# Kernel optimization log

Hardware: AMD Instinct MI355X
Metric: run time of the kernel (lower is better)

Reference implementation:

```python
import jax, jax.numpy as jnp
import numpy as np

HIDDEN = 1024
NUM_HEADS = 16
HEAD_SIZE = HIDDEN // NUM_HEADS
B, S = 2, 2048


def setup_inputs() -> dict:
    key = jax.random.key(0)
    k_x, k_wqkv, k_bqkv, k_wo, k_bo = jax.random.split(key, 5)
    x = jax.random.normal(k_x, (B, S, HIDDEN), dtype=jnp.float32)
    # Dense kernels, fan-in scaled like lecun_normal init
    Wqkv = jax.random.normal(k_wqkv, (HIDDEN, 3 * HIDDEN), dtype=jnp.float32) / np.sqrt(HIDDEN)
    bqkv = jnp.zeros((3 * HIDDEN,), dtype=jnp.float32)
    Wo = jax.random.normal(k_wo, (HIDDEN, HIDDEN), dtype=jnp.float32) / np.sqrt(HIDDEN)
    bo = jnp.zeros((HIDDEN,), dtype=jnp.float32)
    return {"x": x, "Wqkv": Wqkv, "bqkv": bqkv, "Wo": Wo, "bo": bo}


def reference(x, Wqkv, bqkv, Wo, bo):
    b, s, h = x.shape
    qkv = jnp.einsum('bsh,hf->bsf', x, Wqkv) + bqkv          # [b, s, 3*h]
    qkv = qkv.reshape(b, s, 3, NUM_HEADS, HEAD_SIZE)
    q, k, v = qkv[:, :, 0], qkv[:, :, 1], qkv[:, :, 2]        # [b, s, nh, hd]
    scale = 1.0 / np.sqrt(HEAD_SIZE)
    scores = jnp.einsum('bqhd,bkhd->bhqk', q, k) * scale      # [b, nh, s, s]
    weights = jax.nn.softmax(scores, axis=-1)
    attn = jnp.einsum('bhqk,bkhd->bqhd', weights, v)          # [b, s, nh, hd]
    attn = attn.reshape(b, s, h)
    return jnp.einsum('bsh,hf->bsf', attn, Wo) + bo
```

## Files before the change

kernel.cpp:

```cpp
#include <hip/hip_runtime.h>
#include <hip/hip_bf16.h>

#define HIDDEN 1024
#define NH 16
#define BATCH 2
#define SEQ 2048

typedef __attribute__((ext_vector_type(8))) short bf16x8;
typedef __attribute__((ext_vector_type(4))) float f32x4;

__device__ __forceinline__ ushort f2bf(float f) {
    __hip_bfloat16 h = __float2bfloat16(f);
    return *reinterpret_cast<ushort*>(&h);
}
__device__ __forceinline__ float bf2f(ushort u) {
    __hip_bfloat16 h;
    *reinterpret_cast<ushort*>(&h) = u;
    return __bfloat162float(h);
}

__device__ __forceinline__ void async_copy16(const ushort* g, ushort* l) {
    __builtin_amdgcn_global_load_lds((const __attribute__((address_space(1))) void*)g,
                                     (__attribute__((address_space(3))) void*)l,
                                     16, 0, 0);
}

__global__ void prep_kernel(const float* __restrict__ x,
                            const float* __restrict__ Wqkv,
                            const float* __restrict__ Wo,
                            ushort* __restrict__ xb,
                            ushort* __restrict__ Wt,
                            ushort* __restrict__ WoT_hi,
                            ushort* __restrict__ WoT_lo)
{
    __shared__ float t[32][33];
    const int bid = blockIdx.x;
    const int tid = threadIdx.x;

    if (bid < 4096) {
        int i = (bid * 256 + tid) * 4;
        float4 v = *(const float4*)(x + i);
        ushort4 w;
        w.x = f2bf(v.x); w.y = f2bf(v.y); w.z = f2bf(v.z); w.w = f2bf(v.w);
        *(ushort4*)(xb + i) = w;
        return;
    }
    const int r = tid >> 3;
    const int c = (tid & 7) * 4;
    if (bid < 7168) {
        int tt = bid - 4096;
        int k0 = (tt & 31) * 32;
        int n0 = (tt >> 5) * 32;
        const int N = 3 * HIDDEN, K = HIDDEN;
        float4 v = *(const float4*)(Wqkv + (size_t)(k0 + r) * N + n0 + c);
        t[r][c] = v.x; t[r][c + 1] = v.y; t[r][c + 2] = v.z; t[r][c + 3] = v.w;
        __syncthreads();
        ushort4 w;
        w.x = f2bf(t[c + 0][r]); w.y = f2bf(t[c + 1][r]);
        w.z = f2bf(t[c + 2][r]); w.w = f2bf(t[c + 3][r]);
        *(ushort4*)(Wt + (size_t)(n0 + r) * K + k0 + c) = w;
    } else {
        int tt = bid - 7168;
        int k0 = (tt & 31) * 32;
        int n0 = (tt >> 5) * 32;
        const int N = HIDDEN, K = HIDDEN;
        float4 v = *(const float4*)(Wo + (size_t)(k0 + r) * N + n0 + c);
        t[r][c] = v.x; t[r][c + 1] = v.y; t[r][c + 2] = v.z; t[r][c + 3] = v.w;
        __syncthreads();
        ushort4 whi, wlo;
        float vv;
        vv = t[c + 0][r]; whi.x = f2bf(vv); wlo.x = f2bf(vv - bf2f(whi.x));
        vv = t[c + 1][r]; whi.y = f2bf(vv); wlo.y = f2bf(vv - bf2f(whi.y));
        vv = t[c + 2][r]; whi.z = f2bf(vv); wlo.z = f2bf(vv - bf2f(whi.z));
        vv = t[c + 3][r]; whi.w = f2bf(vv); wlo.w = f2bf(vv - bf2f(whi.w));
        *(ushort4*)(WoT_hi + (size_t)(n0 + r) * K + k0 + c) = whi;
        *(ushort4*)(WoT_lo + (size_t)(n0 + r) * K + k0 + c) = wlo;
    }
}

__global__ void transpose_v_kernel(const ushort* __restrict__ qkvb,
                                   ushort* __restrict__ vtg)
{
    __shared__ ushort T[64][72];
    int blk = blockIdx.x;
    int st = blk & 31;
    int h  = (blk >> 5) & 15;
    int b  = blk >> 9;
    int s0 = st * 64;

    int s  = threadIdx.x >> 2;
    int c0 = (threadIdx.x & 3) * 2;
    const ushort* src = qkvb + ((size_t)(b * SEQ + s0 + s)) * 3072 + 2048 + h * 64;
    *(uint4*)&T[s][c0 * 8]     = *(const uint4*)(src + c0 * 8);
    *(uint4*)&T[s][c0 * 8 + 8] = *(const uint4*)(src + c0 * 8 + 8);
    __syncthreads();

    int d = threadIdx.x >> 2;
    ushort* dst = vtg + ((size_t)((b * NH + h) * 64 + d)) * SEQ + s0;
    #pragma unroll
    for (int cc = 0; cc < 2; cc++) {
        int c2 = (threadIdx.x & 3) * 2 + cc;
        ushort tmp[8];
        #pragma unroll
        for (int j = 0; j < 8; j++) {
            int sp = c2 * 8 + j;
            int key = (sp & 3) * 16 + (sp >> 2);
            tmp[j] = T[key][d];
        }
        *(uint4*)(dst + c2 * 8) = *(const uint4*)tmp;
    }
}

__global__ __launch_bounds__(256, 3)
void gemm_mfma_bf16_kernel(const ushort* __restrict__ A,
                           const ushort* __restrict__ Bt,
                           const float* __restrict__ bias,
                           ushort* __restrict__ C, int N,
                           int qscale_cols)
{
    constexpr int K = 1024;
    __shared__ ushort As[128 * 64];
    __shared__ ushort Bs[128 * 64];

    const int tid  = threadIdx.x;
    const int wave = tid >> 6;
    const int lane = tid & 63;
    const int l16  = lane & 15;
    const int quad = lane >> 4;
    const int wm = wave & 1, wn = wave >> 1;

    const int bm = blockIdx.y * 128;
    const int bn = blockIdx.x * 128;

    const int srow = lane >> 3;
    const int lblk = (lane & 7) ^ srow;
    const ushort* Ag = A  + (size_t)(bm + wave * 32 + srow) * K + lblk * 8;
    const ushort* Bg = Bt + (size_t)(bn + wave * 32 + srow) * K + lblk * 8;
    ushort* Asl = As + wave * 32 * 64;
    ushort* Bsl = Bs + wave * 32 * 64;

    f32x4 acc[4][4];
    #pragma unroll
    for (int i = 0; i < 4; i++)
        #pragma unroll
        for (int j = 0; j < 4; j++) acc[i][j] = (f32x4){0.f, 0.f, 0.f, 0.f};

    for (int k0 = 0; k0 < K; k0 += 64) {
        __syncthreads();
        #pragma unroll
        for (int t = 0; t < 4; t++) {
            async_copy16(Ag + (size_t)t * 8 * K + k0, Asl + t * 8 * 64);
            async_copy16(Bg + (size_t)t * 8 * K + k0, Bsl + t * 8 * 64);
        }
        __syncthreads();

        #pragma unroll
        for (int s = 0; s < 2; s++) {
            bf16x8 af[4], bfr[4];
            #pragma unroll
            for (int i = 0; i < 4; i++) {
                int m = wm * 64 + i * 16 + l16;
                int n = wn * 64 + i * 16 + l16;
                af[i]  = *(const bf16x8*)&As[m * 64 + (((s * 4 + quad) ^ (m & 7)) << 3)];
                bfr[i] = *(const bf16x8*)&Bs[n * 64 + (((s * 4 + quad) ^ (n & 7)) << 3)];
            }
            #pragma unroll
            for (int i = 0; i < 4; i++)
                #pragma unroll
                for (int j = 0; j < 4; j++)
                    acc[i][j] = __builtin_amdgcn_mfma_f32_16x16x32_bf16(af[i], bfr[j], acc[i][j], 0, 0, 0);
        }
    }

    #pragma unroll
    for (int j = 0; j < 4; j++) {
        int col = bn + wn * 64 + j * 16 + l16;
        float bv = bias[col];
        float s = (col < qscale_cols) ? 0.125f : 1.0f;
        #pragma unroll
        for (int i = 0; i < 4; i++) {
            int row0 = bm + wm * 64 + i * 16 + quad * 4;
            #pragma unroll
            for (int r = 0; r < 4; r++)
                C[(size_t)(row0 + r) * N + col] = f2bf((acc[i][j][r] + bv) * s);
        }
    }
}

__global__ __launch_bounds__(256, 2)
void gemm3_split_kernel(const ushort* __restrict__ Ahi,
                        const ushort* __restrict__ Alo,
                        const ushort* __restrict__ Bthi,
                        const ushort* __restrict__ Btlo,
                        const float* __restrict__ bias,
                        float* __restrict__ C)
{
    constexpr int K = 1024, N = 1024;
    __shared__ ushort AsHi[128 * 64];
    __shared__ ushort AsLo[128 * 64];
    __shared__ ushort BsHi[64 * 64];
    __shared__ ushort BsLo[64 * 64];

    const int tid  = threadIdx.x;
    const int wave = tid >> 6;
    const int lane = tid & 63;
    const int l16  = lane & 15;
    const int quad = lane >> 4;
    const int wm = wave & 1, wn = wave >> 1;

    const int bm = blockIdx.y * 128;
    const int bn = blockIdx.x * 64;

    const int srow = lane >> 3;
    const int lblk = (lane & 7) ^ srow;
    const size_t aoff = (size_t)(bm + wave * 32 + srow) * K + lblk * 8;
    const size_t boff = (size_t)(bn + wave * 16 + srow) * K + lblk * 8;
    const ushort* AgHi = Ahi + aoff;
    const ushort* AgLo = Alo + aoff;
    const ushort* BgHi = Bthi + boff;
    const ushort* BgLo = Btlo + boff;
    ushort* AslHi = AsHi + wave * 32 * 64;
    ushort* AslLo = AsLo + wave * 32 * 64;
    ushort* BslHi = BsHi + wave * 16 * 64;
    ushort* BslLo = BsLo + wave * 16 * 64;

    f32x4 acc[4][2];
    #pragma unroll
    for (int i = 0; i < 4; i++)
        #pragma unroll
        for (int j = 0; j < 2; j++) acc[i][j] = (f32x4){0.f, 0.f, 0.f, 0.f};

    for (int k0 = 0; k0 < K; k0 += 64) {
        __syncthreads();
        #pragma unroll
        for (int t = 0; t < 4; t++) {
            async_copy16(AgHi + (size_t)t * 8 * K + k0, AslHi + t * 8 * 64);
            async_copy16(AgLo + (size_t)t * 8 * K + k0, AslLo + t * 8 * 64);
        }
        #pragma unroll
        for (int t = 0; t < 2; t++) {
            async_copy16(BgHi + (size_t)t * 8 * K + k0, BslHi + t * 8 * 64);
            async_copy16(BgLo + (size_t)t * 8 * K + k0, BslLo + t * 8 * 64);
        }
        __syncthreads();

        #pragma unroll
        for (int s = 0; s < 2; s++) {
            bf16x8 ah[4], al[4], bh[2], bl[2];
            #pragma unroll
            for (int i = 0; i < 4; i++) {
                int m = wm * 64 + i * 16 + l16;
                int idx = m * 64 + (((s * 4 + quad) ^ (m & 7)) << 3);
                ah[i] = *(const bf16x8*)&AsHi[idx];
                al[i] = *(const bf16x8*)&AsLo[idx];
            }
            #pragma unroll
            for (int j = 0; j < 2; j++) {
                int n = wn * 32 + j * 16 + l16;
                int idx = n * 64 + (((s * 4 + quad) ^ (n & 7)) << 3);
                bh[j] = *(const bf16x8*)&BsHi[idx];
                bl[j] = *(const bf16x8*)&BsLo[idx];
            }
            #pragma unroll
            for (int i = 0; i < 4; i++)
                #pragma unroll
                for (int j = 0; j < 2; j++) {
                    acc[i][j] = __builtin_amdgcn_mfma_f32_16x16x32_bf16(ah[i], bh[j], acc[i][j], 0, 0, 0);
                    acc[i][j] = __builtin_amdgcn_mfma_f32_16x16x32_bf16(ah[i], bl[j], acc[i][j], 0, 0, 0);
                    acc[i][j] = __builtin_amdgcn_mfma_f32_16x16x32_bf16(al[i], bh[j], acc[i][j], 0, 0, 0);
                }
        }
    }

    #pragma unroll
    for (int j = 0; j < 2; j++) {
        int col = bn + wn * 32 + j * 16 + l16;
        float bv = bias[col];
        #pragma unroll
        for (int i = 0; i < 4; i++) {
            int row0 = bm + wm * 64 + i * 16 + quad * 4;
            #pragma unroll
            for (int r = 0; r < 4; r++)
                C[(size_t)(row0 + r) * N + col] = acc[i][j][r] + bv;
        }
    }
}

__global__ __launch_bounds__(256, 2)
void attn_mfma_kernel(const ushort* __restrict__ qkvb,
                      const ushort* __restrict__ vtg,
                      int use_vtg,
                      ushort* __restrict__ attn_hi,
                      ushort* __restrict__ attn_lo)
{
    __shared__ ushort Ks[2][64 * 64];
    __shared__ ushort Vs[2][64 * 64];
    __shared__ ushort Ps[4][32 * 72];

    const int tid  = threadIdx.x;
    const int wave = tid >> 6;
    const int lane = tid & 63;
    const int l16  = lane & 15;
    const int quad = lane >> 4;

    const int qb = blockIdx.x & 15;
    const int bh = blockIdx.x >> 4;
    const int h  = bh & (NH - 1);
    const int b  = bh >> 4;

    const int qbase = qb * 128;
    const int hoff  = h * 64;

    bf16x8 a_q[2][2];
    #pragma unroll
    for (int mg = 0; mg < 2; mg++) {
        int qrow = b * SEQ + qbase + wave * 32 + mg * 16 + l16;
        const ushort* qp = qkvb + (size_t)qrow * 3072 + hoff + quad * 8;
        a_q[mg][0] = *(const bf16x8*)qp;
        a_q[mg][1] = *(const bf16x8*)(qp + 32);
    }

    f32x4 o[2][4];
    f32x4 lacc[2];
    #pragma unroll
    for (int mg = 0; mg < 2; mg++) {
        lacc[mg] = (f32x4){0.f, 0.f, 0.f, 0.f};
        #pragma unroll
        for (int nt = 0; nt < 4; nt++) o[mg][nt] = (f32x4){0.f, 0.f, 0.f, 0.f};
    }

    bf16x8 b_ones;
    #pragma unroll
    for (int j = 0; j < 8; j++) b_ones[j] = (short)0x3f80;

    const ushort* kvb    = qkvb + (size_t)b * SEQ * 3072;
    const ushort* vtg_bh = vtg + (size_t)((b * NH + h) * 64) * SEQ;

    const int srow8 = lane >> 3;
    const int sblk  = lane & 7;
    const int gblk  = (sblk ^ srow8) << 3;
    const ushort* kg = kvb + (size_t)(wave * 16 + srow8) * 3072 + 1024 + hoff + gblk;
    const ushort* vg = vtg_bh + (size_t)(wave * 16 + srow8) * SEQ + gblk;

    if (use_vtg) {
        #pragma unroll
        for (int c = 0; c < 2; c++) {
            async_copy16(kg + (size_t)(c * 8) * 3072, &Ks[0][(wave * 16 + c * 8) * 64]);
            async_copy16(vg + (size_t)(c * 8) * SEQ,  &Vs[0][(wave * 16 + c * 8) * 64]);
        }
    }

    for (int t = 0; t < SEQ / 64; t++) {
        const int k0 = t * 64;
        const int cur = t & 1;

        if (use_vtg) {
            asm volatile("s_waitcnt vmcnt(0)" ::: "memory");
            asm volatile("s_barrier" ::: "memory");
            if (t < SEQ / 64 - 1) {
                const int nk0 = k0 + 64;
                #pragma unroll
                for (int c = 0; c < 2; c++) {
                    async_copy16(kg + (size_t)(nk0 + c * 8) * 3072,
                                 &Ks[cur ^ 1][(wave * 16 + c * 8) * 64]);
                    async_copy16(vg + (size_t)(c * 8) * SEQ + nk0,
                                 &Vs[cur ^ 1][(wave * 16 + c * 8) * 64]);
                }
            }
        } else {
            __syncthreads();
            #pragma unroll
            for (int i = 0; i < 2; i++) {
                int key = (tid >> 3) + 32 * i;
                int blk = tid & 7;
                const ushort* ksrc = kvb + (size_t)(k0 + key) * 3072 + 1024 + hoff + blk * 8;
                uint4 kv = *(const uint4*)ksrc;
                *(uint4*)&Ks[cur][key * 64 + ((blk ^ (key & 7)) << 3)] = kv;
                uint4 vv = *(const uint4*)(ksrc + 1024);
                const ushort* vp = (const ushort*)&vv;
                int pk_ = (key & 15) * 4 + (key >> 4);
                #pragma unroll
                for (int j = 0; j < 8; j++) {
                    int d = blk * 8 + j;
                    Vs[cur][d * 64 + (((pk_ >> 3) ^ (d & 7)) << 3) + (pk_ & 7)] = vp[j];
                }
            }
            __syncthreads();
        }

        f32x4 sc[2][4];
        #pragma unroll
        for (int nt = 0; nt < 4; nt++) {
            int key = nt * 16 + l16;
            bf16x8 bk0 = *(const bf16x8*)&Ks[cur][key * 64 + ((quad ^ (key & 7)) << 3)];
            bf16x8 bk1 = *(const bf16x8*)&Ks[cur][key * 64 + (((4 + quad) ^ (key & 7)) << 3)];
            #pragma unroll
            for (int mg = 0; mg < 2; mg++) {
                f32x4 a = (f32x4){0.f, 0.f, 0.f, 0.f};
                a = __builtin_amdgcn_mfma_f32_16x16x32_bf16(a_q[mg][0], bk0, a, 0, 0, 0);
                a = __builtin_amdgcn_mfma_f32_16x16x32_bf16(a_q[mg][1], bk1, a, 0, 0, 0);
                sc[mg][nt] = a;
            }
        }

        #pragma unroll
        for (int mg = 0; mg < 2; mg++) {
            #pragma unroll
            for (int r = 0; r < 4; r++) {
                int q = mg * 16 + quad * 4 + r;
                uint2 pk2;
                pk2.x = (uint)f2bf(__expf(sc[mg][0][r])) |
                        ((uint)f2bf(__expf(sc[mg][1][r])) << 16);
                pk2.y = (uint)f2bf(__expf(sc[mg][2][r])) |
                        ((uint)f2bf(__expf(sc[mg][3][r])) << 16);
                *(uint2*)&Ps[wave][q * 72 + l16 * 4] = pk2;
            }
        }

        asm volatile("s_waitcnt lgkmcnt(0)" ::: "memory");
        bf16x8 a_p[2][2];
        #pragma unroll
        for (int mg = 0; mg < 2; mg++) {
            a_p[mg][0] = *(const bf16x8*)&Ps[wave][(mg * 16 + l16) * 72 + quad * 8];
            a_p[mg][1] = *(const bf16x8*)&Ps[wave][(mg * 16 + l16) * 72 + 32 + quad * 8];
        }

        #pragma unroll
        for (int nt = 0; nt < 4; nt++) {
            int d = nt * 16 + l16;
            bf16x8 bv0 = *(const bf16x8*)&Vs[cur][d * 64 + ((quad ^ (d & 7)) << 3)];
            bf16x8 bv1 = *(const bf16x8*)&Vs[cur][d * 64 + (((4 + quad) ^ (d & 7)) << 3)];
            #pragma unroll
            for (int mg = 0; mg < 2; mg++) {
                o[mg][nt] = __builtin_amdgcn_mfma_f32_16x16x32_bf16(a_p[mg][0], bv0, o[mg][nt], 0, 0, 0);
                o[mg][nt] = __builtin_amdgcn_mfma_f32_16x16x32_bf16(a_p[mg][1], bv1, o[mg][nt], 0, 0, 0);
            }
        }
        #pragma unroll
        for (int mg = 0; mg < 2; mg++) {
            lacc[mg] = __builtin_amdgcn_mfma_f32_16x16x32_bf16(a_p[mg][0], b_ones, lacc[mg], 0, 0, 0);
            lacc[mg] = __builtin_amdgcn_mfma_f32_16x16x32_bf16(a_p[mg][1], b_ones, lacc[mg], 0, 0, 0);
        }
    }

    #pragma unroll
    for (int mg = 0; mg < 2; mg++) {
        #pragma unroll
        for (int r = 0; r < 4; r++) {
            float inv = 1.f / lacc[mg][r];
            int row = b * SEQ + qbase + wave * 32 + mg * 16 + quad * 4 + r;
            size_t base = (size_t)row * HIDDEN + hoff + l16;
            #pragma unroll
            for (int nt = 0; nt < 4; nt++) {
                float val = o[mg][nt][r] * inv;
                ushort hi = f2bf(val);
                ushort lo = f2bf(val - bf2f(hi));
                attn_hi[base + nt * 16] = hi;
                attn_lo[base + nt * 16] = lo;
            }
        }
    }
}

extern "C" void kernel_launch(void* const* d_in, const int* in_sizes, int n_in,
                              void* d_out, int out_size, void* d_ws, size_t ws_size,
                              hipStream_t stream) {
    const float* x    = (const float*)d_in[0];
    const float* Wqkv = (const float*)d_in[1];
    const float* bqkv = (const float*)d_in[2];
    const float* Wo   = (const float*)d_in[3];
    const float* bo   = (const float*)d_in[4];
    float* out = (float*)d_out;

    const int M = BATCH * SEQ;
    const size_t MB = 1024 * 1024;

    char* ws = (char*)d_ws;
    ushort* qkvb    = (ushort*)ws;
    ushort* attn_hi = (ushort*)(ws + 24 * MB);
    ushort* attn_lo = (ushort*)(ws + 32 * MB);
    ushort* xb      = (ushort*)(ws + 24 * MB);
    ushort* Wt      = (ushort*)(ws + 32 * MB);
    ushort* WoT_hi  = (ushort*)(ws + 40 * MB);
    ushort* WoT_lo  = (ushort*)(ws + 42 * MB);
    ushort* vtg     = (ushort*)(ws + 44 * MB);
    const int use_vtg = (ws_size >= 52 * MB) ? 1 : 0;

    prep_kernel<<<8192, 256, 0, stream>>>(x, Wqkv, Wo, xb, Wt, WoT_hi, WoT_lo);

    {
        dim3 grid((3 * HIDDEN) / 128, M / 128);
        gemm_mfma_bf16_kernel<<<grid, 256, 0, stream>>>(xb, Wt, bqkv, qkvb,
                                                        3 * HIDDEN, HIDDEN);
    }

    if (use_vtg) {
        transpose_v_kernel<<<BATCH * NH * (SEQ / 64), 256, 0, stream>>>(qkvb, vtg);
    }

    attn_mfma_kernel<<<BATCH * NH * (SEQ / 128), 256, 0, stream>>>(qkvb, vtg, use_vtg,
                                                                   attn_hi, attn_lo);

    {
        dim3 grid(HIDDEN / 64, M / 128);
        gemm3_split_kernel<<<grid, 256, 0, stream>>>(attn_hi, attn_lo,
                                                     WoT_hi, WoT_lo, bo, out);
    }
}
```

Baseline: 207.1 us.

## Split attention key range across two wave groups with LDS reduction

The attention kernel now launches 512 threads per block: two groups of four waves each process half of the key sequence for the same 128 queries. Afterwards they combine their partial O and row-sum accumulators through shared memory before normalizing and writing. The aim is to double the number of waves working on each query block, adding latency hiding and parallelism. In exchange it drops the double-buffered async prefetch, adds an extra barrier on every tile plus a final reduction, and raises occupancy demands through launch_bounds(512,4). Using unnormalized exp with no running max is unchanged from before.

```diff
diff --git a/kernel.cpp b/kernel.cpp
--- a/kernel.cpp
+++ b/kernel.cpp
@@ -286,22 +286,22 @@
     }
 }
 
-__global__ __launch_bounds__(256, 2)
+__global__ __launch_bounds__(512, 4)
 void attn_mfma_kernel(const ushort* __restrict__ qkvb,
                       const ushort* __restrict__ vtg,
                       int use_vtg,
                       ushort* __restrict__ attn_hi,
                       ushort* __restrict__ attn_lo)
 {
-    __shared__ ushort Ks[2][64 * 64];
-    __shared__ ushort Vs[2][64 * 64];
-    __shared__ ushort Ps[4][32 * 72];
-
-    const int tid  = threadIdx.x;
-    const int wave = tid >> 6;
-    const int lane = tid & 63;
-    const int l16  = lane & 15;
-    const int quad = lane >> 4;
+    __shared__ __align__(16) ushort smem[34816];
+
+    const int tid   = threadIdx.x;
+    const int wave  = tid >> 6;
+    const int wavel = wave & 3;
+    const int kh    = wave >> 2;
+    const int lane  = tid & 63;
+    const int l16   = lane & 15;
+    const int quad  = lane >> 4;
 
     const int qb = blockIdx.x & 15;
     const int bh = blockIdx.x >> 4;
@@ -311,10 +311,14 @@
     const int qbase = qb * 128;
     const int hoff  = h * 64;
 
+    ushort* KsH = smem + kh * 4096;
+    ushort* VsH = smem + 8192 + kh * 4096;
+    ushort* Psw = smem + 16384 + wave * 2304;
+
     bf16x8 a_q[2][2];
     #pragma unroll
     for (int mg = 0; mg < 2; mg++) {
-        int qrow = b * SEQ + qbase + wave * 32 + mg * 16 + l16;
+        int qrow = b * SEQ + qbase + wavel * 32 + mg * 16 + l16;
         const ushort* qp = qkvb + (size_t)qrow * 3072 + hoff + quad * 8;
         a_q[mg][0] = *(const bf16x8*)qp;
         a_q[mg][1] = *(const bf16x8*)(qp + 32);
@@ -337,63 +341,46 @@
     const ushort* vtg_bh = vtg + (size_t)((b * NH + h) * 64) * SEQ;
 
     const int srow8 = lane >> 3;
-    const int sblk  = lane & 7;
-    const int gblk  = (sblk ^ srow8) << 3;
-    const ushort* kg = kvb + (size_t)(wave * 16 + srow8) * 3072 + 1024 + hoff + gblk;
-    const ushort* vg = vtg_bh + (size_t)(wave * 16 + srow8) * SEQ + gblk;
-
-    if (use_vtg) {
-        #pragma unroll
-        for (int c = 0; c < 2; c++) {
-            async_copy16(kg + (size_t)(c * 8) * 3072, &Ks[0][(wave * 16 + c * 8) * 64]);
-            async_copy16(vg + (size_t)(c * 8) * SEQ,  &Vs[0][(wave * 16 + c * 8) * 64]);
-        }
-    }
-
-    for (int t = 0; t < SEQ / 64; t++) {
+    const int gblk  = ((lane & 7) ^ srow8) << 3;
+    const ushort* kg = kvb + (size_t)(kh * 1024 + wavel * 16 + srow8) * 3072 + 1024 + hoff + gblk;
+    const ushort* vg = vtg_bh + (size_t)(wavel * 16 + srow8) * SEQ + kh * 1024 + gblk;
+
+    for (int t = 0; t < 16; t++) {
         const int k0 = t * 64;
-        const int cur = t & 1;
-
+        __syncthreads();
         if (use_vtg) {
-            asm volatile("s_waitcnt vmcnt(0)" ::: "memory");
-            asm volatile("s_barrier" ::: "memory");
-            if (t < SEQ / 64 - 1) {
-                const int nk0 = k0 + 64;
-                #pragma unroll
-                for (int c = 0; c < 2; c++) {
-                    async_copy16(kg + (size_t)(nk0 + c * 8) * 3072,
-                                 &Ks[cur ^ 1][(wave * 16 + c * 8) * 64]);
-                    async_copy16(vg + (size_t)(c * 8) * SEQ + nk0,
-                                 &Vs[cur ^ 1][(wave * 16 + c * 8) * 64]);
-                }
+            #pragma unroll
+            for (int c = 0; c < 2; c++) {
+                async_copy16(kg + (size_t)(k0 + c * 8) * 3072, KsH + (wavel * 16 + c * 8) * 64);
+                async_copy16(vg + (size_t)(c * 8) * SEQ + k0,  VsH + (wavel * 16 + c * 8) * 64);
             }
         } else {
-            __syncthreads();
+            const int tl = tid & 255;
             #pragma unroll
             for (int i = 0; i < 2; i++) {
-                int key = (tid >> 3) + 32 * i;
-                int blk = tid & 7;
-                const ushort* ksrc = kvb + (size_t)(k0 + key) * 3072 + 1024 + hoff + blk * 8;
+                int key = (tl >> 3) + 32 * i;
+                int blk = tl & 7;
+                const ushort* ksrc = kvb + (size_t)(kh * 1024 + k0 + key) * 3072 + 1024 + hoff + blk * 8;
                 uint4 kv = *(const uint4*)ksrc;
-                *(uint4*)&Ks[cur][key * 64 + ((blk ^ (key & 7)) << 3)] = kv;
+                *(uint4*)&KsH[key * 64 + ((blk ^ (key & 7)) << 3)] = kv;
                 uint4 vv = *(const uint4*)(ksrc + 1024);
                 const ushort* vp = (const ushort*)&vv;
                 int pk_ = (key & 15) * 4 + (key >> 4);
                 #pragma unroll
                 for (int j = 0; j < 8; j++) {
                     int d = blk * 8 + j;
-                    Vs[cur][d * 64 + (((pk_ >> 3) ^ (d & 7)) << 3) + (pk_ & 7)] = vp[j];
+                    VsH[d * 64 + (((pk_ >> 3) ^ (d & 7)) << 3) + (pk_ & 7)] = vp[j];
                 }
             }
-            __syncthreads();
-        }
+        }
+        __syncthreads();
 
         f32x4 sc[2][4];
         #pragma unroll
         for (int nt = 0; nt < 4; nt++) {
             int key = nt * 16 + l16;
-            bf16x8 bk0 = *(const bf16x8*)&Ks[cur][key * 64 + ((quad ^ (key & 7)) << 3)];
-            bf16x8 bk1 = *(const bf16x8*)&Ks[cur][key * 64 + (((4 + quad) ^ (key & 7)) << 3)];
+            bf16x8 bk0 = *(const bf16x8*)&KsH[key * 64 + ((quad ^ (key & 7)) << 3)];
+            bf16x8 bk1 = *(const bf16x8*)&KsH[key * 64 + (((4 + quad) ^ (key & 7)) << 3)];
             #pragma unroll
             for (int mg = 0; mg < 2; mg++) {
                 f32x4 a = (f32x4){0.f, 0.f, 0.f, 0.f};
@@ -413,7 +400,7 @@
                         ((uint)f2bf(__expf(sc[mg][1][r])) << 16);
                 pk2.y = (uint)f2bf(__expf(sc[mg][2][r])) |
                         ((uint)f2bf(__expf(sc[mg][3][r])) << 16);
-                *(uint2*)&Ps[wave][q * 72 + l16 * 4] = pk2;
+                *(uint2*)&Psw[q * 72 + l16 * 4] = pk2;
             }
         }
 
@@ -421,15 +408,15 @@
         bf16x8 a_p[2][2];
         #pragma unroll
         for (int mg = 0; mg < 2; mg++) {
-            a_p[mg][0] = *(const bf16x8*)&Ps[wave][(mg * 16 + l16) * 72 + quad * 8];
-            a_p[mg][1] = *(const bf16x8*)&Ps[wave][(mg * 16 + l16) * 72 + 32 + quad * 8];
+            a_p[mg][0] = *(const bf16x8*)&Psw[(mg * 16 + l16) * 72 + quad * 8];
+            a_p[mg][1] = *(const bf16x8*)&Psw[(mg * 16 + l16) * 72 + 32 + quad * 8];
         }
 
         #pragma unroll
         for (int nt = 0; nt < 4; nt++) {
             int d = nt * 16 + l16;
-            bf16x8 bv0 = *(const bf16x8*)&Vs[cur][d * 64 + ((quad ^ (d & 7)) << 3)];
-            bf16x8 bv1 = *(const bf16x8*)&Vs[cur][d * 64 + (((4 + quad) ^ (d & 7)) << 3)];
+            bf16x8 bv0 = *(const bf16x8*)&VsH[d * 64 + ((quad ^ (d & 7)) << 3)];
+            bf16x8 bv1 = *(const bf16x8*)&VsH[d * 64 + (((4 + quad) ^ (d & 7)) << 3)];
             #pragma unroll
             for (int mg = 0; mg < 2; mg++) {
                 o[mg][nt] = __builtin_amdgcn_mfma_f32_16x16x32_bf16(a_p[mg][0], bv0, o[mg][nt], 0, 0, 0);
@@ -443,20 +430,44 @@
         }
     }
 
-    #pragma unroll
-    for (int mg = 0; mg < 2; mg++) {
-        #pragma unroll
-        for (int r = 0; r < 4; r++) {
-            float inv = 1.f / lacc[mg][r];
-            int row = b * SEQ + qbase + wave * 32 + mg * 16 + quad * 4 + r;
-            size_t base = (size_t)row * HIDDEN + hoff + l16;
-            #pragma unroll
-            for (int nt = 0; nt < 4; nt++) {
-                float val = o[mg][nt][r] * inv;
-                ushort hi = f2bf(val);
-                ushort lo = f2bf(val - bf2f(hi));
-                attn_hi[base + nt * 16] = hi;
-                attn_lo[base + nt * 16] = lo;
+    __syncthreads();
+    float* osc = (float*)smem;
+    float* lsc = (float*)(smem + 16384);
+    const int fo = wavel * 2048 + quad * 64 + l16 * 4;
+    const int fl = wavel * 512 + quad * 64 + l16 * 4;
+    if (kh == 1) {
+        #pragma unroll
+        for (int mg = 0; mg < 2; mg++) {
+            #pragma unroll
+            for (int nt = 0; nt < 4; nt++)
+                *(f32x4*)&osc[fo + (mg * 4 + nt) * 256] = o[mg][nt];
+            *(f32x4*)&lsc[fl + mg * 256] = lacc[mg];
+        }
+    }
+    __syncthreads();
+    if (kh == 0) {
+        #pragma unroll
+        for (int mg = 0; mg < 2; mg++) {
+            #pragma unroll
+            for (int nt = 0; nt < 4; nt++)
+                o[mg][nt] += *(const f32x4*)&osc[fo + (mg * 4 + nt) * 256];
+            lacc[mg] += *(const f32x4*)&lsc[fl + mg * 256];
+        }
+        #pragma unroll
+        for (int mg = 0; mg < 2; mg++) {
+            #pragma unroll
+            for (int r = 0; r < 4; r++) {
+                float inv = 1.f / lacc[mg][r];
+                int row = b * SEQ + qbase + wavel * 32 + mg * 16 + quad * 4 + r;
+                size_t base = (size_t)row * HIDDEN + hoff + l16;
+                #pragma unroll
+                for (int nt = 0; nt < 4; nt++) {
+                    float val = o[mg][nt][r] * inv;
+                    ushort hi = f2bf(val);
+                    ushort lo = f2bf(val - bf2f(hi));
+                    attn_hi[base + nt * 16] = hi;
+                    attn_lo[base + nt * 16] = lo;
+                }
             }
         }
     }
@@ -498,7 +509,7 @@
         transpose_v_kernel<<<BATCH * NH * (SEQ / 64), 256, 0, stream>>>(qkvb, vtg);
     }
 
-    attn_mfma_kernel<<<BATCH * NH * (SEQ / 128), 256, 0, stream>>>(qkvb, vtg, use_vtg,
+    attn_mfma_kernel<<<BATCH * NH * (SEQ / 128), 512, 0, stream>>>(qkvb, vtg, use_vtg,
                                                                    attn_hi, attn_lo);
 
     {
```

Result: faster. 199.6 us (-3.6%).
